# Performance work log

Hardware: AMD Instinct MI355X
Metric: run time of the kernel (lower is better)

Reference implementation:

```python
import jax, jax.numpy as jnp
import numpy as np

B, S, D, H, R = 2, 2048, 1024, 16, 64
DD = D // H  # head depth = 64
EPS = 1e-06


def setup_inputs() -> dict:
    key = jax.random.key(0)
    ks = jax.random.split(key, 12)
    sc = 1.0 / np.sqrt(D)
    inp = {
        'v': jax.random.normal(ks[0], (B, S, D), jnp.float32),
        'k': jax.random.normal(ks[1], (B, S, D), jnp.float32),
        'q': jax.random.normal(ks[2], (B, S, D), jnp.float32),
        'wq_w': jax.random.normal(ks[3], (D, D), jnp.float32) * sc,
        'wq_b': jnp.zeros((D,), jnp.float32),
        'wk_w': jax.random.normal(ks[4], (D, D), jnp.float32) * sc,
        'wk_b': jnp.zeros((D,), jnp.float32),
        'wv_w': jax.random.normal(ks[5], (D, D), jnp.float32) * sc,
        'wv_b': jnp.zeros((D,), jnp.float32),
        'wc_w': jax.random.normal(ks[6], (D, D), jnp.float32) * sc,
        'wc_b': jnp.zeros((D,), jnp.float32),
        # random-feature projection (orthogonal in original; gaussian suffices for a math-equivalent reference)
        'wg': jax.random.normal(ks[7], (H, DD, R), jnp.float32) * (1.0 / np.sqrt(DD)),
    }
    return inp


def _split_heads(x):
    # [B,S,D] -> [B,H,S,DD]
    return x.reshape(B, S, H, DD).transpose(0, 2, 1, 3)


def _combine_heads(x):
    # [B,H,S,DD] -> [B,S,D]
    return x.transpose(0, 2, 1, 3).reshape(B, S, D)


def _sm_approx(x, wg):
    # x: [B,H,S,DD], wg: [H,DD,R] -> phi(x): [B,H,S,R]
    rsqr_d = 1.0 / np.sqrt(DD)
    h_x = jnp.exp(-0.5 * jnp.sum(jnp.square(x), axis=-1, keepdims=True))
    phi_x = rsqr_d * jnp.exp(jnp.einsum('bhsd,hdr->bhsr', x, wg))
    return h_x * phi_x


def reference(v, k, q, wq_w, wq_b, wk_w, wk_b, wv_w, wv_b, wc_w, wc_b, wg):
    norm_d = float(DD) ** -0.25
    qh = _split_heads((q @ wq_w + wq_b) * norm_d)   # [B,H,S,DD]
    kh = _split_heads((k @ wk_w + wk_b) * norm_d)   # [B,H,S,DD]
    vh = _split_heads(v @ wv_w + wv_b)              # [B,H,S,DD]

    q_prime = _sm_approx(qh, wg)                    # [B,H,S,R]
    k_prime = _sm_approx(kh, wg)                    # [B,H,S,R]

    # per-position outer product k_prime (x) v : [B,H,S,R,DD]
    kv_prime = jnp.einsum('bhsr,bhsd->bhsrd', k_prime, vh)

    # causal prefix sums over sequence axis (k_prev/kv_prev = 0 case)
    k_prefix = jnp.cumsum(k_prime, axis=2)          # [B,H,S,R]
    kv_prefix = jnp.cumsum(kv_prime, axis=2)        # [B,H,S,R,DD]

    qk_prefix = jnp.sum(q_prime * k_prefix, axis=-1, keepdims=True)       # [B,H,S,1]
    attn_unnorm = jnp.einsum('bhsr,bhsrd->bhsd', q_prime, kv_prefix)      # [B,H,S,DD]
    attn = attn_unnorm / (EPS + qk_prefix)

    out = _combine_heads(attn) @ wc_w + wc_b        # [B,S,D]
    return (k_prefix, kv_prefix, out)
```

## Files before the change

kernel.cpp:

```cpp
#include <hip/hip_runtime.h>
#include <hip/hip_bf16.h>

#define BB 2
#define SS 2048
#define DD 1024
#define HH 16
#define RR 64
#define DH 64
#define BH (BB*HH)
#define MM (BB*SS)
#define CH 32
#define NCH (SS/CH)
#define CSROW (RR*DH + RR)

using short8 = __attribute__((ext_vector_type(8))) short;
using f32x4  = __attribute__((ext_vector_type(4))) float;

typedef const __attribute__((address_space(1))) unsigned int* gp_t;
typedef __attribute__((address_space(3))) unsigned int* lp_t;

__device__ __forceinline__ void gll16(const void* g, void* l) {
    __builtin_amdgcn_global_load_lds((gp_t)g, (lp_t)l, 16, 0, 0);
}

__global__ __launch_bounds__(256) void k_pre(
    const float* __restrict__ q, const float* __restrict__ k, const float* __restrict__ v,
    const float* __restrict__ bq, const float* __restrict__ bk, const float* __restrict__ bv,
    const float* __restrict__ wq, const float* __restrict__ wk,
    const float* __restrict__ wv, const float* __restrict__ wc,
    __hip_bfloat16* __restrict__ Xb, float* __restrict__ biasb,
    __hip_bfloat16* __restrict__ WT, __hip_bfloat16* __restrict__ wcT)
{
    int z = blockIdx.y;
    __shared__ float tile[64][65];
    if (z < 3) {
        const float* src = (z == 0) ? q : (z == 1) ? k : v;
        size_t i = ((size_t)blockIdx.x * 256 + threadIdx.x) * 4;
        float4 f = *(const float4*)(src + i);
        __hip_bfloat16* dst = Xb + (size_t)z * 4194304 + i;
        dst[0] = __float2bfloat16(f.x);
        dst[1] = __float2bfloat16(f.y);
        dst[2] = __float2bfloat16(f.z);
        dst[3] = __float2bfloat16(f.w);
        if (blockIdx.x == 0 && threadIdx.x < 1024) {
            const float* bb = (z == 0) ? bq : (z == 1) ? bk : bv;
            biasb[z * 1024 + threadIdx.x] = bb[threadIdx.x];
        }
    } else {
        if (blockIdx.x >= 256) return;
        int zz = z - 3;
        const float* W = (zz == 0) ? wq : (zz == 1) ? wk : (zz == 2) ? wv : wc;
        __hip_bfloat16* T = (zz < 3) ? (WT + (size_t)zz * 1048576) : wcT;
        int k0 = (blockIdx.x >> 4) * 64, n0 = (blockIdx.x & 15) * 64;
        for (int i = threadIdx.x; i < 4096; i += 256) {
            int r = i >> 6, cc = i & 63;
            tile[r][cc] = W[(size_t)(k0 + r) * 1024 + n0 + cc];
        }
        __syncthreads();
        for (int i = threadIdx.x; i < 4096; i += 256) {
            int nl = i >> 6, kl = i & 63;
            T[(size_t)(n0 + nl) * 1024 + k0 + kl] = __float2bfloat16(tile[kl][nl]);
        }
    }
}

__global__ __launch_bounds__(256) void gemm_bt(
    const __hip_bfloat16* __restrict__ X, const __hip_bfloat16* __restrict__ WT,
    const float* __restrict__ bias, float* __restrict__ Cout,
    long zsX, long zsW, long zsB, long zsC, int applyNorm)
{
    const int K = 1024, N = 1024;
    int z = blockIdx.z;
    const short* Xz = (const short*)(X + (size_t)z * zsX);
    const short* Wz = (const short*)(WT + (size_t)z * zsW);
    const float* bz = bias + (size_t)z * zsB;
    float* Cz = Cout + (size_t)z * zsC;
    float scale = (applyNorm && z < 2) ? 0.35355339059327373f : 1.0f;

    __shared__ short As[128 * 32];
    __shared__ short Bs[128 * 32];
    int tid = threadIdx.x;
    int m0 = blockIdx.y * 128;
    int n0 = blockIdx.x * 128;
    int lane = tid & 63;
    int w = tid >> 6;
    int wm = (w >> 1) * 64, wn = (w & 1) * 64;

    f32x4 acc[4][4] = {};

    int srow = tid >> 2;
    int scol = (tid & 3) * 8;
    const short* Ag = Xz + (size_t)(m0 + srow) * K + scol;
    const short* Bg = Wz + (size_t)(n0 + srow) * K + scol;
    short* lA0 = As + tid * 8;
    short* lA1 = As + 64 * 32 + tid * 8;
    short* lB0 = Bs + tid * 8;
    short* lB1 = Bs + 64 * 32 + tid * 8;

    int fr = lane & 15, kg = (lane >> 4) * 8;

    for (int kt = 0; kt < K / 32; ++kt) {
        __syncthreads();
        gll16(Ag + kt * 32, lA0);
        gll16(Ag + (size_t)64 * K + kt * 32, lA1);
        gll16(Bg + kt * 32, lB0);
        gll16(Bg + (size_t)64 * K + kt * 32, lB1);
        __syncthreads();

        short8 af[4], bf[4];
#pragma unroll
        for (int mi = 0; mi < 4; ++mi)
            af[mi] = *(const short8*)&As[(wm + mi * 16 + fr) * 32 + kg];
#pragma unroll
        for (int ni = 0; ni < 4; ++ni)
            bf[ni] = *(const short8*)&Bs[(wn + ni * 16 + fr) * 32 + kg];
#pragma unroll
        for (int mi = 0; mi < 4; ++mi)
#pragma unroll
            for (int ni = 0; ni < 4; ++ni)
                acc[mi][ni] = __builtin_amdgcn_mfma_f32_16x16x32_bf16(af[mi], bf[ni], acc[mi][ni], 0, 0, 0);
    }

    int rg = (lane >> 4) * 4;
#pragma unroll
    for (int mi = 0; mi < 4; ++mi)
#pragma unroll
        for (int ni = 0; ni < 4; ++ni) {
            int gn = n0 + wn + ni * 16 + fr;
            float bval = bz[gn];
#pragma unroll
            for (int i = 0; i < 4; ++i) {
                int gm = m0 + wm + mi * 16 + rg + i;
                Cz[(size_t)gm * N + gn] = (acc[mi][ni][i] + bval) * scale;
            }
        }
}

__global__ __launch_bounds__(256) void k_phi(
    const float* __restrict__ qh, const float* __restrict__ kh,
    const float* __restrict__ wg,
    float* __restrict__ qprime, float* __restrict__ kprime)
{
    int z = blockIdx.z;
    int bh = blockIdx.y;
    int b = bh >> 4, h = bh & 15;
    int s0 = blockIdx.x * 64;
    int tid = threadIdx.x, lane = tid & 63, w = tid >> 6;
    const float* X = (z == 0) ? qh : kh;
    float* O = (z == 0) ? qprime : kprime;

    float wgc[DH];
#pragma unroll
    for (int dd = 0; dd < DH; ++dd)
        wgc[dd] = wg[((size_t)h * DH + dd) * RR + lane];

    __shared__ float xs[64][DH];
    for (int i = tid; i < 64 * DH; i += 256) {
        int rr = i >> 6, dd = i & 63;
        xs[rr][dd] = X[((size_t)b * SS + s0 + rr) * DD + h * DH + dd];
    }
    __syncthreads();

    for (int rr = w; rr < 64; rr += 4) {
        float arg = 0.f, nrm = 0.f;
#pragma unroll
        for (int d4 = 0; d4 < 16; ++d4) {
            float4 xq = *(const float4*)&xs[rr][d4 * 4];
            arg += xq.x * wgc[d4 * 4 + 0] + xq.y * wgc[d4 * 4 + 1]
                 + xq.z * wgc[d4 * 4 + 2] + xq.w * wgc[d4 * 4 + 3];
            nrm += xq.x * xq.x + xq.y * xq.y + xq.z * xq.z + xq.w * xq.w;
        }
        O[((size_t)bh * SS + s0 + rr) * RR + lane] = 0.125f * __expf(arg - 0.5f * nrm);
    }
}

__global__ __launch_bounds__(64) void k_chunksum(
    const float* __restrict__ kprime, const float* __restrict__ vh,
    float* __restrict__ cs)
{
    int c = blockIdx.x;
    int bh = blockIdx.y;
    int b = bh >> 4, h = bh & 15;
    int lane = threadIdx.x;
    __shared__ float kp[CH][RR];
    size_t rowbase = (size_t)bh * SS + c * CH;
    for (int i = 0; i < CH; ++i)
        kp[i][lane] = kprime[(rowbase + i) * RR + lane];
    __syncthreads();

    float st[RR];
#pragma unroll
    for (int r = 0; r < RR; ++r) st[r] = 0.f;
    float kpsum = 0.f;
    const float* vptr = vh + ((size_t)b * SS + c * CH) * DD + h * DH + lane;
    for (int s = 0; s < CH; ++s) {
        float vd = vptr[(size_t)s * DD];
        kpsum += kp[s][lane];
#pragma unroll
        for (int rq = 0; rq < RR / 4; ++rq) {
            float4 kq = *(const float4*)&kp[s][rq * 4];
            st[rq * 4 + 0] += kq.x * vd;
            st[rq * 4 + 1] += kq.y * vd;
            st[rq * 4 + 2] += kq.z * vd;
            st[rq * 4 + 3] += kq.w * vd;
        }
    }
    float* out = cs + (size_t)(bh * NCH + c) * CSROW;
#pragma unroll
    for (int r = 0; r < RR; ++r) out[r * 64 + lane] = st[r];
    out[4096 + lane] = kpsum;
}

__global__ __launch_bounds__(256) void k_scan(float* __restrict__ cs)
{
    int t = blockIdx.x * 256 + threadIdx.x;
    if (t >= BH * CSROW) return;
    int bh = t / CSROW;
    int e = t - bh * CSROW;
    float* p = cs + (size_t)bh * NCH * CSROW + e;
    float v[NCH];
#pragma unroll
    for (int c = 0; c < NCH; ++c) v[c] = p[(size_t)c * CSROW];
    float run = 0.f;
#pragma unroll
    for (int c = 0; c < NCH; ++c) {
        float x = v[c];
        p[(size_t)c * CSROW] = run;
        run += x;
    }
}

__global__ __launch_bounds__(64) void k_scanfinal(
    const float* __restrict__ kprime, const float* __restrict__ qprime,
    const float* __restrict__ vh, const float* __restrict__ cs,
    float* __restrict__ kp_out, float* __restrict__ kv_out,
    __hip_bfloat16* __restrict__ attnb)
{
    int c = blockIdx.x;
    int bh = blockIdx.y;
    int b = bh >> 4, h = bh & 15;
    int lane = threadIdx.x;
    __shared__ float kp[CH][RR];
    __shared__ float qp[CH][RR];
    size_t rowbase = (size_t)bh * SS + c * CH;
    for (int i = 0; i < CH; ++i) {
        kp[i][lane] = kprime[(rowbase + i) * RR + lane];
        qp[i][lane] = qprime[(rowbase + i) * RR + lane];
    }
    __syncthreads();

    const float* off = cs + (size_t)(bh * NCH + c) * CSROW;
    float st[RR];
#pragma unroll
    for (int r = 0; r < RR; ++r) st[r] = off[r * 64 + lane];
    float kps = off[4096 + lane];

    const float* vptr = vh + ((size_t)b * SS + c * CH) * DD + h * DH + lane;
    for (int s = 0; s < CH; ++s) {
        float vd = vptr[(size_t)s * DD];
        kps += kp[s][lane];
        size_t srow = rowbase + s;
        kp_out[srow * RR + lane] = kps;

        float qksum = qp[s][lane] * kps;
#pragma unroll
        for (int m = 1; m < 64; m <<= 1) qksum += __shfl_xor(qksum, m, 64);

        float accd = 0.f;
        float* kvp = kv_out + srow * (size_t)(RR * DH) + lane;
#pragma unroll
        for (int rq = 0; rq < RR / 4; ++rq) {
            float4 kq = *(const float4*)&kp[s][rq * 4];
            float4 qq = *(const float4*)&qp[s][rq * 4];
            st[rq * 4 + 0] += kq.x * vd; accd += qq.x * st[rq * 4 + 0];
            __builtin_nontemporal_store(st[rq * 4 + 0], kvp + (rq * 4 + 0) * 64);
            st[rq * 4 + 1] += kq.y * vd; accd += qq.y * st[rq * 4 + 1];
            __builtin_nontemporal_store(st[rq * 4 + 1], kvp + (rq * 4 + 1) * 64);
            st[rq * 4 + 2] += kq.z * vd; accd += qq.z * st[rq * 4 + 2];
            __builtin_nontemporal_store(st[rq * 4 + 2], kvp + (rq * 4 + 2) * 64);
            st[rq * 4 + 3] += kq.w * vd; accd += qq.w * st[rq * 4 + 3];
            __builtin_nontemporal_store(st[rq * 4 + 3], kvp + (rq * 4 + 3) * 64);
        }
        float attn = accd / (1e-6f + qksum);
        int s_abs = c * CH + s;
        attnb[((size_t)b * SS + s_abs) * DD + h * DH + lane] = __float2bfloat16(attn);
    }
}

extern "C" void kernel_launch(void* const* d_in, const int* in_sizes, int n_in,
                              void* d_out, int out_size, void* d_ws, size_t ws_size,
                              hipStream_t stream) {
    const float* v_in  = (const float*)d_in[0];
    const float* k_in  = (const float*)d_in[1];
    const float* q_in  = (const float*)d_in[2];
    const float* wq_w  = (const float*)d_in[3];
    const float* wq_b  = (const float*)d_in[4];
    const float* wk_w  = (const float*)d_in[5];
    const float* wk_b  = (const float*)d_in[6];
    const float* wv_w  = (const float*)d_in[7];
    const float* wv_b  = (const float*)d_in[8];
    const float* wc_w  = (const float*)d_in[9];
    const float* wc_b  = (const float*)d_in[10];
    const float* wg    = (const float*)d_in[11];

    char* ws = (char*)d_ws;
    __hip_bfloat16* Xb    = (__hip_bfloat16*)(ws + 0);
    __hip_bfloat16* WT    = (__hip_bfloat16*)(ws + 25165824);
    __hip_bfloat16* wcT   = (__hip_bfloat16*)(ws + 31457280);
    float* biasb          = (float*)(ws + 33554432);
    float* qhkv           = (float*)(ws + 33570816);
    float* qprime         = (float*)(ws + 83902464);
    float* kprime         = (float*)(ws + 100679680);
    float* cs             = (float*)(ws + 117456896);
    __hip_bfloat16* attnb = (__hip_bfloat16*)(ws + 151535616);

    float* kp_out = (float*)d_out;
    float* kv_out = kp_out + 4194304;
    float* out_o  = kv_out + 268435456;

    k_pre<<<dim3(4096, 7), 256, 0, stream>>>(q_in, k_in, v_in, wq_b, wk_b, wv_b,
                                             wq_w, wk_w, wv_w, wc_w, Xb, biasb, WT, wcT);
    gemm_bt<<<dim3(8, 32, 3), 256, 0, stream>>>(Xb, WT, biasb, qhkv,
                                                4194304L, 1048576L, 1024L, 4194304L, 1);
    k_phi<<<dim3(32, 32, 2), 256, 0, stream>>>(qhkv, qhkv + 4194304, wg, qprime, kprime);
    k_chunksum<<<dim3(NCH, BH), 64, 0, stream>>>(kprime, qhkv + 2 * 4194304, cs);
    k_scan<<<dim3(520), 256, 0, stream>>>(cs);
    k_scanfinal<<<dim3(NCH, BH), 64, 0, stream>>>(kprime, qprime, qhkv + 2 * 4194304, cs,
                                                  kp_out, kv_out, attnb);
    gemm_bt<<<dim3(8, 32, 1), 256, 0, stream>>>(attnb, wcT, wc_b, out_o, 0L, 0L, 0L, 0L, 0);
}
```

Before: 393.5 us.

## Fuse random-feature projection into QK GEMM epilogue and vectorize scan-final stores

Removes the separate k_phi kernel. The Q/K projection GEMM epilogue now normalizes its tile in place, writes it as bf16 to LDS, and runs a small MFMA against a pre-transposed bf16 wg to produce q'/k' directly. This avoids writing and re-reading the full fp32 qh/kh tensors. The scan-final kernel is restructured so each lane handles 4 contiguous d values with float4 kv stores and a cross-group shuffle reduction. This trades bf16 rounding in the phi projection (precision risk before exp) and extra epilogue LDS use for less memory traffic.

```diff
diff --git a/kernel.cpp b/kernel.cpp
--- a/kernel.cpp
+++ b/kernel.cpp
@@ -23,13 +23,20 @@
     __builtin_amdgcn_global_load_lds((gp_t)g, (lp_t)l, 16, 0, 0);
 }
 
+__device__ __forceinline__ unsigned short f2bf(float x) {
+    __hip_bfloat16 h = __float2bfloat16(x);
+    return *(unsigned short*)&h;
+}
+
 __global__ __launch_bounds__(256) void k_pre(
     const float* __restrict__ q, const float* __restrict__ k, const float* __restrict__ v,
     const float* __restrict__ bq, const float* __restrict__ bk, const float* __restrict__ bv,
     const float* __restrict__ wq, const float* __restrict__ wk,
     const float* __restrict__ wv, const float* __restrict__ wc,
+    const float* __restrict__ wg,
     __hip_bfloat16* __restrict__ Xb, float* __restrict__ biasb,
-    __hip_bfloat16* __restrict__ WT, __hip_bfloat16* __restrict__ wcT)
+    __hip_bfloat16* __restrict__ WT, __hip_bfloat16* __restrict__ wcT,
+    short* __restrict__ wgbT)
 {
     int z = blockIdx.y;
     __shared__ float tile[64][65];
@@ -42,11 +49,12 @@
         dst[1] = __float2bfloat16(f.y);
         dst[2] = __float2bfloat16(f.z);
         dst[3] = __float2bfloat16(f.w);
-        if (blockIdx.x == 0 && threadIdx.x < 1024) {
+        if (blockIdx.x == 0) {
             const float* bb = (z == 0) ? bq : (z == 1) ? bk : bv;
-            biasb[z * 1024 + threadIdx.x] = bb[threadIdx.x];
-        }
-    } else {
+            for (int t = threadIdx.x; t < 1024; t += 256)
+                biasb[z * 1024 + t] = bb[t];
+        }
+    } else if (z < 7) {
         if (blockIdx.x >= 256) return;
         int zz = z - 3;
         const float* W = (zz == 0) ? wq : (zz == 1) ? wk : (zz == 2) ? wv : wc;
@@ -61,13 +69,25 @@
             int nl = i >> 6, kl = i & 63;
             T[(size_t)(n0 + nl) * 1024 + k0 + kl] = __float2bfloat16(tile[kl][nl]);
         }
+    } else {
+        if (blockIdx.x >= 16) return;
+        int hx = blockIdx.x;
+        for (int i = threadIdx.x; i < 4096; i += 256)
+            tile[i >> 6][i & 63] = wg[(size_t)hx * 4096 + i];
+        __syncthreads();
+        for (int i = threadIdx.x; i < 4096; i += 256) {
+            int r = i >> 6, d = i & 63;
+            wgbT[(size_t)hx * 4096 + r * 64 + d] = (short)f2bf(tile[d][r]);
+        }
     }
 }
 
 __global__ __launch_bounds__(256) void gemm_bt(
     const __hip_bfloat16* __restrict__ X, const __hip_bfloat16* __restrict__ WT,
     const float* __restrict__ bias, float* __restrict__ Cout,
-    long zsX, long zsW, long zsB, long zsC, int applyNorm)
+    const short* __restrict__ wgbT,
+    float* __restrict__ qp_out, float* __restrict__ kp_out2,
+    long zsX, long zsW, long zsB, long zsC, int mode)
 {
     const int K = 1024, N = 1024;
     int z = blockIdx.z;
@@ -75,10 +95,13 @@
     const short* Wz = (const short*)(WT + (size_t)z * zsW);
     const float* bz = bias + (size_t)z * zsB;
     float* Cz = Cout + (size_t)z * zsC;
-    float scale = (applyNorm && z < 2) ? 0.35355339059327373f : 1.0f;
-
-    __shared__ short As[128 * 32];
-    __shared__ short Bs[128 * 32];
+
+    __shared__ short smem[18432];
+    short* As = smem;
+    short* Bs = smem + 4096;
+    short* wgT = smem;
+    short* xw  = smem + 9216;
+
     int tid = threadIdx.x;
     int m0 = blockIdx.y * 128;
     int n0 = blockIdx.x * 128;
@@ -121,7 +144,95 @@
                 acc[mi][ni] = __builtin_amdgcn_mfma_f32_16x16x32_bf16(af[mi], bf[ni], acc[mi][ni], 0, 0, 0);
     }
 
-    int rg = (lane >> 4) * 4;
+    int g = lane >> 4, c4 = lane & 15;
+
+    if (mode == 1 && z < 2) {
+        const float nd = 0.35355339059327373f;
+        float* O = (z == 0) ? qp_out : kp_out2;
+        int h = blockIdx.x * 2 + (w & 1);
+        int b = m0 >> 11;
+        float bias_n[4];
+#pragma unroll
+        for (int ni = 0; ni < 4; ++ni) bias_n[ni] = bz[n0 + wn + ni * 16 + c4];
+
+        __syncthreads();
+        {
+            int row = tid >> 2, part = tid & 3;
+#pragma unroll
+            for (int hl = 0; hl < 2; ++hl) {
+                const short* src = wgbT + ((size_t)(blockIdx.x * 2 + hl)) * 4096 + row * 64 + part * 16;
+                short8 v0 = *(const short8*)src;
+                short8 v1 = *(const short8*)(src + 8);
+                *(short8*)&wgT[hl * 4608 + row * 72 + part * 16] = v0;
+                *(short8*)&wgT[hl * 4608 + row * 72 + part * 16 + 8] = v1;
+            }
+        }
+        __syncthreads();
+
+        short* xww = xw + w * 2304;
+        const short* wgh = wgT + (w & 1) * 4608;
+
+#pragma unroll
+        for (int pass = 0; pass < 2; ++pass) {
+            float nrm[2][4];
+#pragma unroll
+            for (int mi_l = 0; mi_l < 2; ++mi_l) {
+                int mi = pass * 2 + mi_l;
+                float part_n[4] = {0.f, 0.f, 0.f, 0.f};
+#pragma unroll
+                for (int ni = 0; ni < 4; ++ni)
+#pragma unroll
+                    for (int i = 0; i < 4; ++i) {
+                        float xv = (acc[mi][ni][i] + bias_n[ni]) * nd;
+                        part_n[i] += xv * xv;
+                        xww[(mi_l * 16 + g * 4 + i) * 72 + ni * 16 + c4] = (short)f2bf(xv);
+                    }
+#pragma unroll
+                for (int i = 0; i < 4; ++i) {
+                    float t = part_n[i];
+                    t += __shfl_xor(t, 1, 64);
+                    t += __shfl_xor(t, 2, 64);
+                    t += __shfl_xor(t, 4, 64);
+                    t += __shfl_xor(t, 8, 64);
+                    nrm[mi_l][i] = t;
+                }
+            }
+            short8 afr[2][2], bfr[4][2];
+#pragma unroll
+            for (int mi_l = 0; mi_l < 2; ++mi_l)
+#pragma unroll
+                for (int kk = 0; kk < 2; ++kk)
+                    afr[mi_l][kk] = *(const short8*)&xww[(mi_l * 16 + c4) * 72 + kk * 32 + g * 8];
+#pragma unroll
+            for (int ri = 0; ri < 4; ++ri)
+#pragma unroll
+                for (int kk = 0; kk < 2; ++kk)
+                    bfr[ri][kk] = *(const short8*)&wgh[(ri * 16 + c4) * 72 + kk * 32 + g * 8];
+            f32x4 p[2][4] = {};
+#pragma unroll
+            for (int mi_l = 0; mi_l < 2; ++mi_l)
+#pragma unroll
+                for (int ri = 0; ri < 4; ++ri)
+#pragma unroll
+                    for (int kk = 0; kk < 2; ++kk)
+                        p[mi_l][ri] = __builtin_amdgcn_mfma_f32_16x16x32_bf16(afr[mi_l][kk], bfr[ri][kk], p[mi_l][ri], 0, 0, 0);
+#pragma unroll
+            for (int mi_l = 0; mi_l < 2; ++mi_l)
+#pragma unroll
+                for (int ri = 0; ri < 4; ++ri)
+#pragma unroll
+                    for (int i = 0; i < 4; ++i) {
+                        int mi = pass * 2 + mi_l;
+                        float val = 0.125f * __expf(p[mi_l][ri][i] - 0.5f * nrm[mi_l][i]);
+                        int row = m0 + wm + mi * 16 + g * 4 + i;
+                        int s = row & 2047;
+                        O[((size_t)(b * 16 + h) * SS + s) * RR + ri * 16 + c4] = val;
+                    }
+        }
+        return;
+    }
+
+    int rg = g * 4;
 #pragma unroll
     for (int mi = 0; mi < 4; ++mi)
 #pragma unroll
@@ -131,47 +242,9 @@
 #pragma unroll
             for (int i = 0; i < 4; ++i) {
                 int gm = m0 + wm + mi * 16 + rg + i;
-                Cz[(size_t)gm * N + gn] = (acc[mi][ni][i] + bval) * scale;
+                Cz[(size_t)gm * N + gn] = acc[mi][ni][i] + bval;
             }
         }
-}
-
-__global__ __launch_bounds__(256) void k_phi(
-    const float* __restrict__ qh, const float* __restrict__ kh,
-    const float* __restrict__ wg,
-    float* __restrict__ qprime, float* __restrict__ kprime)
-{
-    int z = blockIdx.z;
-    int bh = blockIdx.y;
-    int b = bh >> 4, h = bh & 15;
-    int s0 = blockIdx.x * 64;
-    int tid = threadIdx.x, lane = tid & 63, w = tid >> 6;
-    const float* X = (z == 0) ? qh : kh;
-    float* O = (z == 0) ? qprime : kprime;
-
-    float wgc[DH];
-#pragma unroll
-    for (int dd = 0; dd < DH; ++dd)
-        wgc[dd] = wg[((size_t)h * DH + dd) * RR + lane];
-
-    __shared__ float xs[64][DH];
-    for (int i = tid; i < 64 * DH; i += 256) {
-        int rr = i >> 6, dd = i & 63;
-        xs[rr][dd] = X[((size_t)b * SS + s0 + rr) * DD + h * DH + dd];
-    }
-    __syncthreads();
-
-    for (int rr = w; rr < 64; rr += 4) {
-        float arg = 0.f, nrm = 0.f;
-#pragma unroll
-        for (int d4 = 0; d4 < 16; ++d4) {
-            float4 xq = *(const float4*)&xs[rr][d4 * 4];
-            arg += xq.x * wgc[d4 * 4 + 0] + xq.y * wgc[d4 * 4 + 1]
-                 + xq.z * wgc[d4 * 4 + 2] + xq.w * wgc[d4 * 4 + 3];
-            nrm += xq.x * xq.x + xq.y * xq.y + xq.z * xq.z + xq.w * xq.w;
-        }
-        O[((size_t)bh * SS + s0 + rr) * RR + lane] = 0.125f * __expf(arg - 0.5f * nrm);
-    }
 }
 
 __global__ __launch_bounds__(64) void k_chunksum(
@@ -240,6 +313,7 @@
     int bh = blockIdx.y;
     int b = bh >> 4, h = bh & 15;
     int lane = threadIdx.x;
+    int g = lane >> 4, c4 = lane & 15;
     __shared__ float kp[CH][RR];
     __shared__ float qp[CH][RR];
     size_t rowbase = (size_t)bh * SS + c * CH;
@@ -250,15 +324,16 @@
     __syncthreads();
 
     const float* off = cs + (size_t)(bh * NCH + c) * CSROW;
-    float st[RR];
-#pragma unroll
-    for (int r = 0; r < RR; ++r) st[r] = off[r * 64 + lane];
+    f32x4 st[16];
+#pragma unroll
+    for (int j = 0; j < 16; ++j)
+        st[j] = *(const f32x4*)&off[(4 * j + g) * 64 + 4 * c4];
     float kps = off[4096 + lane];
 
-    const float* vptr = vh + ((size_t)b * SS + c * CH) * DD + h * DH + lane;
+    const float* vrow = vh + ((size_t)b * SS + c * CH) * DD + h * DH;
     for (int s = 0; s < CH; ++s) {
-        float vd = vptr[(size_t)s * DD];
-        kps += kp[s][lane];
+        float kpl = kp[s][lane];
+        kps += kpl;
         size_t srow = rowbase + s;
         kp_out[srow * RR + lane] = kps;
 
@@ -266,24 +341,31 @@
 #pragma unroll
         for (int m = 1; m < 64; m <<= 1) qksum += __shfl_xor(qksum, m, 64);
 
-        float accd = 0.f;
-        float* kvp = kv_out + srow * (size_t)(RR * DH) + lane;
-#pragma unroll
-        for (int rq = 0; rq < RR / 4; ++rq) {
-            float4 kq = *(const float4*)&kp[s][rq * 4];
-            float4 qq = *(const float4*)&qp[s][rq * 4];
-            st[rq * 4 + 0] += kq.x * vd; accd += qq.x * st[rq * 4 + 0];
-            __builtin_nontemporal_store(st[rq * 4 + 0], kvp + (rq * 4 + 0) * 64);
-            st[rq * 4 + 1] += kq.y * vd; accd += qq.y * st[rq * 4 + 1];
-            __builtin_nontemporal_store(st[rq * 4 + 1], kvp + (rq * 4 + 1) * 64);
-            st[rq * 4 + 2] += kq.z * vd; accd += qq.z * st[rq * 4 + 2];
-            __builtin_nontemporal_store(st[rq * 4 + 2], kvp + (rq * 4 + 2) * 64);
-            st[rq * 4 + 3] += kq.w * vd; accd += qq.w * st[rq * 4 + 3];
-            __builtin_nontemporal_store(st[rq * 4 + 3], kvp + (rq * 4 + 3) * 64);
-        }
-        float attn = accd / (1e-6f + qksum);
-        int s_abs = c * CH + s;
-        attnb[((size_t)b * SS + s_abs) * DD + h * DH + lane] = __float2bfloat16(attn);
+        f32x4 v4 = *(const f32x4*)(vrow + (size_t)s * DD + 4 * c4);
+        f32x4 accp = {0.f, 0.f, 0.f, 0.f};
+        float* kvp = kv_out + srow * (size_t)(RR * DH);
+#pragma unroll
+        for (int j = 0; j < 16; ++j) {
+            float kpj = kp[s][4 * j + g];
+            float qpj = qp[s][4 * j + g];
+            st[j] += kpj * v4;
+            __builtin_nontemporal_store(st[j], (f32x4*)(kvp + (4 * j + g) * 64 + 4 * c4));
+            accp += qpj * st[j];
+        }
+#pragma unroll
+        for (int e = 0; e < 4; ++e) {
+            accp[e] += __shfl_xor(accp[e], 16, 64);
+            accp[e] += __shfl_xor(accp[e], 32, 64);
+        }
+        float rs = 1.0f / (1e-6f + qksum);
+        if (g == 0) {
+            ushort4 pkt;
+            pkt.x = f2bf(accp[0] * rs);
+            pkt.y = f2bf(accp[1] * rs);
+            pkt.z = f2bf(accp[2] * rs);
+            pkt.w = f2bf(accp[3] * rs);
+            *(ushort4*)((unsigned short*)attnb + ((size_t)b * SS + c * CH + s) * DD + h * DH + 4 * c4) = pkt;
+        }
     }
 }
 
@@ -313,19 +395,22 @@
     float* kprime         = (float*)(ws + 100679680);
     float* cs             = (float*)(ws + 117456896);
     __hip_bfloat16* attnb = (__hip_bfloat16*)(ws + 151535616);
+    short* wgbT           = (short*)(ws + 159924224);
 
     float* kp_out = (float*)d_out;
     float* kv_out = kp_out + 4194304;
     float* out_o  = kv_out + 268435456;
-
-    k_pre<<<dim3(4096, 7), 256, 0, stream>>>(q_in, k_in, v_in, wq_b, wk_b, wv_b,
-                                             wq_w, wk_w, wv_w, wc_w, Xb, biasb, WT, wcT);
-    gemm_bt<<<dim3(8, 32, 3), 256, 0, stream>>>(Xb, WT, biasb, qhkv,
+    float* vh     = qhkv + 2 * 4194304;
+
+    k_pre<<<dim3(4096, 8), 256, 0, stream>>>(q_in, k_in, v_in, wq_b, wk_b, wv_b,
+                                             wq_w, wk_w, wv_w, wc_w, wg,
+                                             Xb, biasb, WT, wcT, wgbT);
+    gemm_bt<<<dim3(8, 32, 3), 256, 0, stream>>>(Xb, WT, biasb, qhkv, wgbT, qprime, kprime,
                                                 4194304L, 1048576L, 1024L, 4194304L, 1);
-    k_phi<<<dim3(32, 32, 2), 256, 0, stream>>>(qhkv, qhkv + 4194304, wg, qprime, kprime);
-    k_chunksum<<<dim3(NCH, BH), 64, 0, stream>>>(kprime, qhkv + 2 * 4194304, cs);
+    k_chunksum<<<dim3(NCH, BH), 64, 0, stream>>>(kprime, vh, cs);
     k_scan<<<dim3(520), 256, 0, stream>>>(cs);
-    k_scanfinal<<<dim3(NCH, BH), 64, 0, stream>>>(kprime, qprime, qhkv + 2 * 4194304, cs,
+    k_scanfinal<<<dim3(NCH, BH), 64, 0, stream>>>(kprime, qprime, vh, cs,
                                                   kp_out, kv_out, attnb);
-    gemm_bt<<<dim3(8, 32, 1), 256, 0, stream>>>(attnb, wcT, wc_b, out_o, 0L, 0L, 0L, 0L, 0);
-}
+    gemm_bt<<<dim3(8, 32, 1), 256, 0, stream>>>(attnb, wcT, wc_b, out_o, wgbT, qprime, kprime,
+                                                0L, 0L, 0L, 0L, 0);
+}
```

Result: faster. 350.4 us (-10.9%).
